# Optimization experiments

Hardware: AMD Instinct MI355X
Metric: run time of the kernel (lower is better)

Reference implementation:

```python
import jax, jax.numpy as jnp
import numpy as np

B, N, C_IN, C_OUT, K = 2, 2048, 64, 128, 3
SCALE = 12.0  # spread points over ~12^3 unit voxels (voxel_size = 1.0 in the module)


def setup_inputs() -> dict:
    key = jax.random.key(0)
    k1, k2, k3 = jax.random.split(key, 3)
    points = jax.random.uniform(k1, (B, N, 3), dtype=jnp.float32) * SCALE
    features = jax.random.normal(k2, (B, N, C_IN), dtype=jnp.float32)
    # kaiming-uniform-ish init for weight viewed as (K^3*Cin, Cout)
    fan_in = K * K * K * C_IN
    bound = np.sqrt(6.0 / fan_in)
    weight = jax.random.uniform(k3, (K, K, K, C_IN, C_OUT), dtype=jnp.float32,
                                minval=-bound, maxval=bound)
    bias = jnp.zeros((C_OUT,), dtype=jnp.float32)
    return {"points": points, "features": features, "weight": weight, "bias": bias}


def reference(points, features, weight, bias):
    """Sparse 3D conv over a unit voxel grid.

    For each point i, every point j whose voxel index differs by an offset
    within the KxKxK stencil contributes features[j] @ weight[rel_offset].
    Vectorized as: per-offset boolean match matrix (B,N,N) -> masked
    feature aggregation -> one GEMM with that offset's (Cin,Cout) kernel slice.
    """
    k = weight.shape[0]
    c = k // 2
    # torch's .long() truncates toward zero; jnp astype(int32) does the same for floats
    vox = points.astype(jnp.int32)  # (B, N, 3)
    out = jnp.zeros(features.shape[:2] + (weight.shape[-1],), dtype=features.dtype)
    for oi in range(k):
        for oj in range(k):
            for ok in range(k):
                off = jnp.array([oi - c, oj - c, ok - c], dtype=jnp.int32)
                target = vox + off  # voxel that neighbor j must occupy for center i
                # mask[b, i, j] = all(vox[b, j] == vox[b, i] + off)
                mask = jnp.all(vox[:, None, :, :] == target[:, :, None, :], axis=-1)
                agg = jnp.einsum('bij,bjc->bic', mask.astype(features.dtype), features)
                out = out + agg @ weight[oi, oj, ok]  # (B,N,Cin)@(Cin,Cout)
    return out + bias
```

## Files before the change

### kernel.cpp

```cpp
#include <hip/hip_runtime.h>

#define BATCH 2
#define NPTS  2048
#define CIN   64
#define COUT  128
#define GD    14
#define GD2   (GD*GD)
#define NCELL (GD*GD*GD)
#define M     (BATCH*NPTS)
#define VOXF  (BATCH*NCELL*CIN)
#define WTEL  (27*COUT*CIN)

typedef __bf16 bf16x8 __attribute__((ext_vector_type(8)));
typedef float  f32x4  __attribute__((ext_vector_type(4)));
typedef unsigned short us8 __attribute__((ext_vector_type(8)));

__device__ __forceinline__ unsigned short f2bf(float f) {
    unsigned u = __builtin_bit_cast(unsigned, f);
    return (unsigned short)((u + 0x7FFFu + ((u >> 16) & 1u)) >> 16);
}

__global__ __launch_bounds__(256) void k_prep(const float* __restrict__ points,
                                              const float* __restrict__ feat,
                                              const float* __restrict__ weight,
                                              float* __restrict__ voxgrid,
                                              unsigned short* __restrict__ wT,
                                              const unsigned* __restrict__ sentinel_p) {
    const int i = blockIdx.x * 256 + threadIdx.x;
    const unsigned sbits = *sentinel_p;

    if (i < M*CIN) {
        const int g   = i >> 6;
        const int cin = i & 63;
        const int b   = g >> 11;
        const int vx = (int)points[g*3 + 0];
        const int vy = (int)points[g*3 + 1];
        const int vz = (int)points[g*3 + 2];
        const int cell = (vx + 1)*GD2 + (vy + 1)*GD + (vz + 1);
        float* addr = &voxgrid[((size_t)b*NCELL + cell)*CIN + cin];
        const float val = feat[i];
        const unsigned old = atomicCAS((unsigned*)addr, sbits,
                                       __builtin_bit_cast(unsigned, val));
        if (old != sbits) atomicAdd(addr, val);
    }

    const int j = i - M*CIN;
    if (j >= 0 && j < WTEL/4) {
        const int off = j >> 11;
        const int n   = j & 127;
        const int kg  = (j >> 7) & 15;
        const float* wsrc = weight + off*8192 + (kg*4)*128 + n;
        unsigned long long pk =
              (unsigned long long)f2bf(wsrc[0])
            | ((unsigned long long)f2bf(wsrc[128]) << 16)
            | ((unsigned long long)f2bf(wsrc[256]) << 32)
            | ((unsigned long long)f2bf(wsrc[384]) << 48);
        *(unsigned long long*)&wT[(size_t)off*8192 + n*64 + kg*4] = pk;
    }
}

__global__ __launch_bounds__(256, 2) void k_gemm(const float* __restrict__ points,
                                                 const float* __restrict__ voxgrid,
                                                 const unsigned short* __restrict__ wT,
                                                 const float* __restrict__ bias,
                                                 float* __restrict__ out,
                                                 const unsigned* __restrict__ sentinel_p) {
    static constexpr int DELTA[27] = {
        -211,-210,-209,-197,-196,-195,-183,-182,-181,
         -15, -14, -13,  -1,   0,   1,  13,  14,  15,
         181, 182, 183, 195, 196, 197, 209, 210, 211 };

    __shared__ __align__(16) unsigned short Abuf[27*16*64];

    const int t   = threadIdx.x;
    const int bid = blockIdx.x;
    const unsigned sbits = *sentinel_p;

    const int tile = bid & 255;
    const int half = bid >> 8;
    const int g0   = tile * 16;
    const int b    = g0 >> 11;
    const int l    = t & 63;
    const int w    = t >> 6;
    const int q    = l >> 4;
    const int col  = l & 15;
    const int n0   = half * 64 + w * 16;
    const unsigned short* wt = wT + (size_t)(n0 + col)*CIN + q*8;

    us8 bv[4][2];
    #pragma unroll
    for (int s = 0; s < 4; ++s) {
        bv[s][0] = *(const us8*)(wt + s*8192);
        bv[s][1] = *(const us8*)(wt + s*8192 + 32);
    }
    const float bs = bias[n0 + col];

    const int srow = t >> 4;
    const int sc4  = (t & 15) * 4;
    const int pr   = g0 + srow;
    const int svx  = (int)points[pr*3 + 0];
    const int svy  = (int)points[pr*3 + 1];
    const int svz  = (int)points[pr*3 + 2];
    const int scell = (svx + 1)*GD2 + (svy + 1)*GD + (svz + 1);
    const float* sbase = voxgrid + ((size_t)b*NCELL + scell)*CIN + sc4;

    #pragma unroll
    for (int oo = 0; oo < 27; ++oo) {
        const uint4 vb = *(const uint4*)(sbase + DELTA[oo]*CIN);
        const float x = (vb.x == sbits) ? 0.f : __builtin_bit_cast(float, vb.x);
        const float y = (vb.y == sbits) ? 0.f : __builtin_bit_cast(float, vb.y);
        const float z = (vb.z == sbits) ? 0.f : __builtin_bit_cast(float, vb.z);
        const float u = (vb.w == sbits) ? 0.f : __builtin_bit_cast(float, vb.w);
        ushort4 pk;
        pk.x = f2bf(x); pk.y = f2bf(y); pk.z = f2bf(z); pk.w = f2bf(u);
        const int vr   = oo*16 + srow;
        const int byte = vr*128 + ((sc4*2) ^ ((vr & 7) << 4));
        *(ushort4*)((char*)Abuf + byte) = pk;
    }
    __syncthreads();

    f32x4 acc = {0.f, 0.f, 0.f, 0.f};
    #pragma unroll
    for (int oo = 0; oo < 27; ++oo) {
        const int vr   = oo*16 + col;
        const int base = vr*128;
        const int sw   = (vr & 7) << 4;
        us8 a0 = *(const us8*)((char*)Abuf + base + ((q*16)      ^ sw));
        us8 a1 = *(const us8*)((char*)Abuf + base + ((q*16 + 64) ^ sw));
        const int slot = oo & 3;
        us8 b0 = bv[slot][0], b1 = bv[slot][1];
        if (oo < 23) {
            bv[slot][0] = *(const us8*)(wt + (oo+4)*8192);
            bv[slot][1] = *(const us8*)(wt + (oo+4)*8192 + 32);
        }
        acc = __builtin_amdgcn_mfma_f32_16x16x32_bf16(
                  __builtin_bit_cast(bf16x8, a0), __builtin_bit_cast(bf16x8, b0), acc, 0, 0, 0);
        acc = __builtin_amdgcn_mfma_f32_16x16x32_bf16(
                  __builtin_bit_cast(bf16x8, a1), __builtin_bit_cast(bf16x8, b1), acc, 0, 0, 0);
    }

    #pragma unroll
    for (int r = 0; r < 4; ++r)
        out[(size_t)(g0 + q*4 + r)*COUT + n0 + col] = acc[r] + bs;
}

extern "C" void kernel_launch(void* const* d_in, const int* in_sizes, int n_in,
                              void* d_out, int out_size, void* d_ws, size_t ws_size,
                              hipStream_t stream) {
    (void)in_sizes; (void)n_in; (void)out_size;
    const float* points   = (const float*)d_in[0];
    const float* features = (const float*)d_in[1];
    const float* weight   = (const float*)d_in[2];
    const float* bias     = (const float*)d_in[3];
    float* out = (float*)d_out;

    char* ws = (char*)d_ws;
    float*          voxgrid = (float*)ws;           ws += (size_t)VOXF*4;
    unsigned short* wTp     = (unsigned short*)ws;

    const unsigned* sentinel_p =
        (const unsigned*)((char*)d_ws + ((ws_size & ~(size_t)63) - 64));

    const int nscatter = M*CIN/256;
    const int ntrans   = (WTEL/4 + 255)/256;
    k_prep<<<nscatter + ntrans, 256, 0, stream>>>(points, features, weight,
                                                  voxgrid, wTp, sentinel_p);
    k_gemm<<<512, 256, 0, stream>>>(points, voxgrid, wTp, bias, out, sentinel_p);
}
```

Measured before the change: 79.42 us.

## Merge column halves into 512-thread GEMM blocks and shrink prep grid

The GEMM kernel now uses 256 blocks of 512 threads. Each block covers all 128 output columns for 16 points, so the 27-offset gather into shared memory is built once per tile instead of twice, with the gather split across two thread halves. The prep kernel now uses 512 blocks: each thread scatters two feature elements, and the same threads also do the weight transpose. This removes duplicated gather work and shrinks the launch grid, but leaves fewer, larger GEMM blocks, which may lower occupancy and parallelism across CUs.

```diff
diff --git a/kernel.cpp b/kernel.cpp
--- a/kernel.cpp
+++ b/kernel.cpp
@@ -26,10 +26,12 @@
                                               float* __restrict__ voxgrid,
                                               unsigned short* __restrict__ wT,
                                               const unsigned* __restrict__ sentinel_p) {
-    const int i = blockIdx.x * 256 + threadIdx.x;
+    const int tid = blockIdx.x * 256 + threadIdx.x;
     const unsigned sbits = *sentinel_p;
 
-    if (i < M*CIN) {
+    #pragma unroll
+    for (int it = 0; it < 2; ++it) {
+        const int i   = it*(512*256) + tid;
         const int g   = i >> 6;
         const int cin = i & 63;
         const int b   = g >> 11;
@@ -44,11 +46,10 @@
         if (old != sbits) atomicAdd(addr, val);
     }
 
-    const int j = i - M*CIN;
-    if (j >= 0 && j < WTEL/4) {
-        const int off = j >> 11;
-        const int n   = j & 127;
-        const int kg  = (j >> 7) & 15;
+    if (tid < WTEL/4) {
+        const int off = tid >> 11;
+        const int n   = tid & 127;
+        const int kg  = (tid >> 7) & 15;
         const float* wsrc = weight + off*8192 + (kg*4)*128 + n;
         unsigned long long pk =
               (unsigned long long)f2bf(wsrc[0])
@@ -59,7 +60,7 @@
     }
 }
 
-__global__ __launch_bounds__(256, 2) void k_gemm(const float* __restrict__ points,
+__global__ __launch_bounds__(512, 2) void k_gemm(const float* __restrict__ points,
                                                  const float* __restrict__ voxgrid,
                                                  const unsigned short* __restrict__ wT,
                                                  const float* __restrict__ bias,
@@ -76,15 +77,13 @@
     const int bid = blockIdx.x;
     const unsigned sbits = *sentinel_p;
 
-    const int tile = bid & 255;
-    const int half = bid >> 8;
-    const int g0   = tile * 16;
-    const int b    = g0 >> 11;
-    const int l    = t & 63;
-    const int w    = t >> 6;
-    const int q    = l >> 4;
-    const int col  = l & 15;
-    const int n0   = half * 64 + w * 16;
+    const int g0  = bid * 16;
+    const int b   = g0 >> 11;
+    const int l   = t & 63;
+    const int w   = t >> 6;
+    const int q   = l >> 4;
+    const int col = l & 15;
+    const int n0  = w * 16;
     const unsigned short* wt = wT + (size_t)(n0 + col)*CIN + q*8;
 
     us8 bv[4][2];
@@ -95,8 +94,10 @@
     }
     const float bs = bias[n0 + col];
 
-    const int srow = t >> 4;
-    const int sc4  = (t & 15) * 4;
+    const int p    = t >> 8;
+    const int th   = t & 255;
+    const int srow = th >> 4;
+    const int sc4  = (th & 15) * 4;
     const int pr   = g0 + srow;
     const int svx  = (int)points[pr*3 + 0];
     const int svy  = (int)points[pr*3 + 1];
@@ -105,17 +106,20 @@
     const float* sbase = voxgrid + ((size_t)b*NCELL + scell)*CIN + sc4;
 
     #pragma unroll
-    for (int oo = 0; oo < 27; ++oo) {
-        const uint4 vb = *(const uint4*)(sbase + DELTA[oo]*CIN);
-        const float x = (vb.x == sbits) ? 0.f : __builtin_bit_cast(float, vb.x);
-        const float y = (vb.y == sbits) ? 0.f : __builtin_bit_cast(float, vb.y);
-        const float z = (vb.z == sbits) ? 0.f : __builtin_bit_cast(float, vb.z);
-        const float u = (vb.w == sbits) ? 0.f : __builtin_bit_cast(float, vb.w);
-        ushort4 pk;
-        pk.x = f2bf(x); pk.y = f2bf(y); pk.z = f2bf(z); pk.w = f2bf(u);
-        const int vr   = oo*16 + srow;
-        const int byte = vr*128 + ((sc4*2) ^ ((vr & 7) << 4));
-        *(ushort4*)((char*)Abuf + byte) = pk;
+    for (int k2 = 0; k2 < 14; ++k2) {
+        const int oo = p + 2*k2;
+        if (oo < 27) {
+            const uint4 vb = *(const uint4*)(sbase + DELTA[oo]*CIN);
+            const float x = (vb.x == sbits) ? 0.f : __builtin_bit_cast(float, vb.x);
+            const float y = (vb.y == sbits) ? 0.f : __builtin_bit_cast(float, vb.y);
+            const float z = (vb.z == sbits) ? 0.f : __builtin_bit_cast(float, vb.z);
+            const float u = (vb.w == sbits) ? 0.f : __builtin_bit_cast(float, vb.w);
+            ushort4 pk;
+            pk.x = f2bf(x); pk.y = f2bf(y); pk.z = f2bf(z); pk.w = f2bf(u);
+            const int vr   = oo*16 + srow;
+            const int byte = vr*128 + ((sc4*2) ^ ((vr & 7) << 4));
+            *(ushort4*)((char*)Abuf + byte) = pk;
+        }
     }
     __syncthreads();
 
@@ -161,9 +165,6 @@
     const unsigned* sentinel_p =
         (const unsigned*)((char*)d_ws + ((ws_size & ~(size_t)63) - 64));
 
-    const int nscatter = M*CIN/256;
-    const int ntrans   = (WTEL/4 + 255)/256;
-    k_prep<<<nscatter + ntrans, 256, 0, stream>>>(points, features, weight,
-                                                  voxgrid, wTp, sentinel_p);
-    k_gemm<<<512, 256, 0, stream>>>(points, voxgrid, wTp, bias, out, sentinel_p);
+    k_prep<<<512, 256, 0, stream>>>(points, features, weight, voxgrid, wTp, sentinel_p);
+    k_gemm<<<256, 512, 0, stream>>>(points, voxgrid, wTp, bias, out, sentinel_p);
 }
```

New measurement: 80.15 us. About the same (+0.9%).
